# Optimization experiments

Measured on AMD Instinct MI355X. Metric: run time of the kernel, lower is better.

Reference implementation:

```python
import jax, jax.numpy as jnp
import numpy as np

NUM_HEADS = 16
NEG_INF = -1e30  # finite large negative; avoids NaN on fully-masked padded query rows


def setup_inputs() -> dict:
    key = jax.random.key(0)
    k0, k1, k2, k3 = jax.random.split(key, 4)
    B, S, E = 4, 2048, 1024
    x_padded = jax.random.normal(k0, (B, S, E), dtype=jnp.float32)
    # variable lengths in [S//2, S] so no batch row is fully empty
    seq_lengths = jax.random.randint(k1, (B,), S // 2, S + 1).astype(jnp.int32)
    Wqkv = jax.random.normal(k2, (3 * E, E), dtype=jnp.float32) * 0.02  # torch Linear weight [out,in]
    Wout = jax.random.normal(k3, (E, E), dtype=jnp.float32) * 0.02
    return {"x_padded": x_padded, "Wqkv": Wqkv, "Wout": Wout,
            "seq_lengths": seq_lengths, "window_left": 512, "window_right": 0}


def _build_mask(seq_lengths, S, window_left, window_right):
    # key-side padding mask: [B, S]
    pad = jnp.arange(S)[None, :] < seq_lengths[:, None]
    mask = pad[:, None, None, :]  # [B,1,1,S]
    if window_left >= 0 or window_right >= 0:
        i = jnp.arange(S)[:, None]
        j = jnp.arange(S)[None, :]
        win = jnp.ones((S, S), dtype=bool)
        if window_left >= 0:
            win = win & (j >= i - window_left)
        if window_right >= 0:
            win = win & (j <= i + window_right)
        mask = mask & win[None, None, :, :]
    elif (window_left, window_right) == (-1, 0):
        causal = jnp.tril(jnp.ones((S, S), dtype=bool))
        mask = mask & causal[None, None, :, :]
    return mask  # [B,1,S,S] (broadcasts over heads)


def reference(x_padded, Wqkv, Wout, seq_lengths, window_left, window_right):
    B, S, E = x_padded.shape
    H = NUM_HEADS
    D = E // H
    scale = 1.0 / jnp.sqrt(jnp.float32(D))
    qkv = x_padded @ Wqkv.T  # [B,S,3E]
    q, k, v = jnp.split(qkv, 3, axis=-1)
    q = q.reshape(B, S, H, D).transpose(0, 2, 1, 3)  # [B,H,S,D]
    k = k.reshape(B, S, H, D).transpose(0, 2, 1, 3)
    v = v.reshape(B, S, H, D).transpose(0, 2, 1, 3)
    mask = _build_mask(seq_lengths, S, window_left, window_right)
    scores = jnp.einsum("bhid,bhjd->bhij", q, k) * scale
    scores = jnp.where(mask, scores, NEG_INF)
    attn = jax.nn.softmax(scores, axis=-1)
    out = jnp.einsum("bhij,bhjd->bhid", attn, v)  # [B,H,S,D]
    out = out.transpose(0, 2, 1, 3).reshape(B, S, E)
    return out @ Wout.T
```

## Files before the change

kernel.cpp:

```cpp
#include <hip/hip_runtime.h>

typedef __bf16 bf16;
typedef __attribute__((ext_vector_type(2))) __bf16 bf16x2;
typedef __attribute__((ext_vector_type(4))) __bf16 bf16x4;
typedef __attribute__((ext_vector_type(8))) __bf16 bf16x8;
typedef __attribute__((ext_vector_type(4))) float f32x4;
typedef __attribute__((ext_vector_type(16))) float f32x16;

#define B_ 4
#define S_ 2048
#define H_ 16
#define D_ 64
#define E_ 1024

__device__ __forceinline__ int imin(int a, int b) { return a < b ? a : b; }
__device__ __forceinline__ int imax(int a, int b) { return a > b ? a : b; }

__device__ __forceinline__ void gload_lds16(const void* g, void* l) {
  __builtin_amdgcn_global_load_lds(
      (const __attribute__((address_space(1))) void*)g,
      (__attribute__((address_space(3))) void*)l, 16, 0, 0);
}

__global__ __launch_bounds__(256) void f32_to_bf16_kernel(
    const float* __restrict__ in, bf16* __restrict__ out, int n) {
  int i = (blockIdx.x * 256 + threadIdx.x) * 8;
  const int stride = gridDim.x * 256 * 8;
  for (; i < n; i += stride) {
    float4 v0 = *(const float4*)(in + i);
    float4 v1 = *(const float4*)(in + i + 4);
    bf16x8 o;
    o[0] = (bf16)v0.x; o[1] = (bf16)v0.y; o[2] = (bf16)v0.z; o[3] = (bf16)v0.w;
    o[4] = (bf16)v1.x; o[5] = (bf16)v1.y; o[6] = (bf16)v1.z; o[7] = (bf16)v1.w;
    *(bf16x8*)(out + i) = o;
  }
}

__global__ __launch_bounds__(256) void gemm_nt(
    const bf16* __restrict__ A, const bf16* __restrict__ Bm,
    int M, int N, int K, int mode,
    bf16* __restrict__ qd, bf16* __restrict__ kd, bf16* __restrict__ vtd,
    float* __restrict__ outf) {
  __shared__ __align__(16) bf16 As[128 * 64];
  __shared__ __align__(16) bf16 Bs[128 * 64];
  const int tid = threadIdx.x;
  const int wave = tid >> 6, lane = tid & 63;
  const int l15 = lane & 15, l4 = lane >> 4;
  const int tn = blockIdx.x, tm = blockIdx.y;
  const int wm = (wave >> 1) * 64, wn = (wave & 1) * 64;

  f32x4 acc[4][4];
#pragma unroll
  for (int i = 0; i < 4; ++i)
#pragma unroll
    for (int j = 0; j < 4; ++j)
#pragma unroll
      for (int r = 0; r < 4; ++r) acc[i][j][r] = 0.f;

  const bf16* Abase = A + (size_t)tm * 128 * K;
  const bf16* Bbase = Bm + (size_t)tn * 128 * K;

  for (int k0 = 0; k0 < K; k0 += 64) {
#pragma unroll
    for (int it = 0; it < 4; ++it) {
      const int gidx = it * 256 + tid;
      const int row = gidx >> 3, c = gidx & 7;
      const int csw = c ^ (row & 7);
      gload_lds16(Abase + (size_t)row * K + k0 + csw * 8,
                  As + (size_t)(it * 256 + wave * 64) * 8);
      gload_lds16(Bbase + (size_t)row * K + k0 + csw * 8,
                  Bs + (size_t)(it * 256 + wave * 64) * 8);
    }
    __syncthreads();
#pragma unroll
    for (int kc = 0; kc < 2; ++kc) {
      bf16x8 af[4], bfr[4];
#pragma unroll
      for (int i = 0; i < 4; ++i) {
        const int ra = wm + i * 16 + l15;
        af[i] = *(const bf16x8*)(As + ra * 64 + (((kc * 4 + l4) ^ (ra & 7)) * 8));
        const int rb = wn + i * 16 + l15;
        bfr[i] = *(const bf16x8*)(Bs + rb * 64 + (((kc * 4 + l4) ^ (rb & 7)) * 8));
      }
#pragma unroll
      for (int i = 0; i < 4; ++i)
#pragma unroll
        for (int j = 0; j < 4; ++j)
          acc[i][j] = __builtin_amdgcn_mfma_f32_16x16x32_bf16(af[i], bfr[j],
                                                              acc[i][j], 0, 0, 0);
    }
    __syncthreads();
  }

  if (mode == 0) {
#pragma unroll
    for (int i = 0; i < 4; ++i) {
      const int m0 = tm * 128 + wm + i * 16 + l4 * 4;
      const int b = m0 >> 11, s = m0 & (S_ - 1);
#pragma unroll
      for (int j = 0; j < 4; ++j) {
        const int n = tn * 128 + wn + j * 16 + l15;
        const int which = n >> 10;
        const int hn = n & 1023;
        const int h = hn >> 6, d = hn & 63;
        const f32x4 a = acc[i][j];
        if (which == 0) {
#pragma unroll
          for (int r = 0; r < 4; ++r)
            qd[((size_t)(b * H_ + h) * S_ + (s + r)) * D_ + d] =
                (bf16)(a[r] * 0.125f);
        } else if (which == 1) {
#pragma unroll
          for (int r = 0; r < 4; ++r)
            kd[((size_t)(b * H_ + h) * S_ + (s + r)) * D_ + d] = (bf16)a[r];
        } else {
          bf16x4 pv;
#pragma unroll
          for (int r = 0; r < 4; ++r) pv[r] = (bf16)a[r];
          *(bf16x4*)(vtd + ((size_t)(b * H_ + h) * D_ + d) * S_ + s) = pv;
        }
      }
    }
  } else {
#pragma unroll
    for (int i = 0; i < 4; ++i) {
      const int m0 = tm * 128 + wm + i * 16 + l4 * 4;
#pragma unroll
      for (int j = 0; j < 4; ++j) {
        const int n = tn * 128 + wn + j * 16 + l15;
#pragma unroll
        for (int r = 0; r < 4; ++r) outf[(size_t)(m0 + r) * N + n] = acc[i][j][r];
      }
    }
  }
}

__global__ __launch_bounds__(256) void meanv_kernel(const bf16* __restrict__ vt,
                                                    float* __restrict__ meanv) {
  __shared__ float part[256];
  const int bh = blockIdx.x;
  const int tid = threadIdx.x;
  const int d = tid & 63, seg = tid >> 6;
  const bf16* row = vt + ((size_t)bh * D_ + d) * S_ + seg * 512;
  float s = 0.f;
  for (int i = 0; i < 512; i += 8) {
    bf16x8 v = *(const bf16x8*)(row + i);
#pragma unroll
    for (int j = 0; j < 8; ++j) s += (float)v[j];
  }
  part[tid] = s;
  __syncthreads();
  if (tid < 64) {
    float t = part[tid] + part[64 + tid] + part[128 + tid] + part[192 + tid];
    meanv[(size_t)bh * D_ + tid] = t * (1.0f / (float)S_);
  }
}

__device__ __forceinline__ int pk2(float a, float b) {
  union { bf16x2 h; int i; } u;
  u.h[0] = (bf16)a; u.h[1] = (bf16)b;
  return u.i;
}

__global__ __launch_bounds__(256) void attn_kernel(
    const bf16* __restrict__ q, const bf16* __restrict__ k,
    const bf16* __restrict__ vt, const float* __restrict__ meanv,
    const int* __restrict__ seq_lengths, const int* __restrict__ wlp,
    const int* __restrict__ wrp, bf16* __restrict__ attn_out) {
  const int tid = threadIdx.x, wave = tid >> 6, lane = tid & 63;
  const int l31 = lane & 31, l5 = lane >> 5;
  const int bid = blockIdx.x;
  const int bh = bid >> 4;
  const int g = bid & 15;
  const int b = bh >> 4, h = bh & 15;
  const int q0w = g * 128 + wave * 32;
  const int seq_len = seq_lengths[b];
  const int wl = wlp[0], wr = wrp[0];

  const bf16* qbase = q + (size_t)bh * S_ * D_;
  const bf16* kbase = k + (size_t)bh * S_ * D_;
  const bf16* vtb = vt + (size_t)bh * D_ * S_;

  bf16x8 qa[4];
#pragma unroll
  for (int dg = 0; dg < 4; ++dg)
    qa[dg] = *(const bf16x8*)(qbase + (size_t)(q0w + l31) * D_ + dg * 16 + l5 * 8);

  const int hi_ = (wr >= 0) ? imin(q0w + 31 + wr, S_ - 1) : (S_ - 1);
  const int kv_end = imin(hi_ + 1, seq_len);
  const int lo_ = (wl >= 0) ? imax(0, q0w - wl) : 0;
  const int kv_begin = lo_ & ~31;

  f32x16 o0, o1;
#pragma unroll
  for (int r = 0; r < 16; ++r) { o0[r] = 0.f; o1[r] = 0.f; }
  float mrun = -1e30f, lrun = 0.f;

  for (int kt = kv_begin; kt < kv_end; kt += 32) {
    f32x16 sf;
#pragma unroll
    for (int r = 0; r < 16; ++r) sf[r] = 0.f;
#pragma unroll
    for (int dg = 0; dg < 4; ++dg) {
      bf16x8 kb = *(const bf16x8*)(kbase + (size_t)(kt + l31) * D_ + dg * 16 + l5 * 8);
      sf = __builtin_amdgcn_mfma_f32_32x32x16_bf16(kb, qa[dg], sf, 0, 0, 0);
    }

    bool allv = (kt + 31 < seq_len);
    if (wr >= 0) allv = allv && (kt + 31 <= q0w + wr);
    if (wl >= 0) allv = allv && (kt >= q0w + 31 - wl);

    float p[16];
    float tmax = -1e30f;
    if (allv) {
#pragma unroll
      for (int r = 0; r < 16; ++r) { p[r] = sf[r]; tmax = fmaxf(tmax, p[r]); }
    } else {
      const int qrow = q0w + l31;
#pragma unroll
      for (int r = 0; r < 16; ++r) {
        const int key = kt + (r & 3) + 8 * (r >> 2) + 4 * l5;
        bool valid = (key < seq_len);
        if (wr >= 0) valid = valid && (key <= qrow + wr);
        if (wl >= 0) valid = valid && (key >= qrow - wl);
        p[r] = valid ? sf[r] : -1e30f;
        tmax = fmaxf(tmax, p[r]);
      }
    }
    tmax = fmaxf(tmax, __shfl_xor(tmax, 32, 64));

    if (!__all(tmax <= mrun + 8.0f)) {
      const float mnew = fmaxf(mrun, tmax);
      const float corr = __expf(mrun - mnew);
      mrun = mnew;
      lrun *= corr;
#pragma unroll
      for (int r = 0; r < 16; ++r) { o0[r] *= corr; o1[r] *= corr; }
    }

    float lsum = 0.f;
#pragma unroll
    for (int r = 0; r < 16; ++r) {
      const float pe = (p[r] <= -1e29f) ? 0.f : __expf(p[r] - mrun);
      p[r] = pe;
      lsum += pe;
    }
    lsum += __shfl_xor(lsum, 32, 64);
    lrun += lsum;

    bf16x8 pb[2];
#pragma unroll
    for (int kg = 0; kg < 2; ++kg) {
      const int w0 = pk2(p[kg * 8 + 0], p[kg * 8 + 1]);
      const int w1 = pk2(p[kg * 8 + 2], p[kg * 8 + 3]);
      const int w2 = pk2(p[kg * 8 + 4], p[kg * 8 + 5]);
      const int w3 = pk2(p[kg * 8 + 6], p[kg * 8 + 7]);
      auto r02 = __builtin_amdgcn_permlane32_swap(w0, w2, false, false);
      auto r13 = __builtin_amdgcn_permlane32_swap(w1, w3, false, false);
      union { int i[4]; bf16x8 v; } u;
      u.i[0] = r02[0]; u.i[1] = r13[0]; u.i[2] = r02[1]; u.i[3] = r13[1];
      pb[kg] = u.v;
    }

#pragma unroll
    for (int kg = 0; kg < 2; ++kg) {
      bf16x8 v0 = *(const bf16x8*)(vtb + (size_t)(l31) * S_ + kt + kg * 16 + l5 * 8);
      bf16x8 v1 = *(const bf16x8*)(vtb + (size_t)(32 + l31) * S_ + kt + kg * 16 + l5 * 8);
      o0 = __builtin_amdgcn_mfma_f32_32x32x16_bf16(v0, pb[kg], o0, 0, 0, 0);
      o1 = __builtin_amdgcn_mfma_f32_32x32x16_bf16(v1, pb[kg], o1, 0, 0, 0);
    }
  }

  const int qrow = q0w + l31;
  bf16* outp = attn_out + ((size_t)(b * S_ + qrow)) * E_ + h * 64;
  if (lrun > 0.f) {
    const float inv = 1.0f / lrun;
#pragma unroll
    for (int dg2 = 0; dg2 < 2; ++dg2) {
      const f32x16& o = dg2 ? o1 : o0;
#pragma unroll
      for (int rg = 0; rg < 4; ++rg) {
        const int d0 = dg2 * 32 + 8 * rg + 4 * l5;
        bf16x4 ov;
#pragma unroll
        for (int j = 0; j < 4; ++j) ov[j] = (bf16)(o[rg * 4 + j] * inv);
        *(bf16x4*)(outp + d0) = ov;
      }
    }
  } else {
    const float* mv = meanv + (size_t)bh * D_;
#pragma unroll
    for (int dg2 = 0; dg2 < 2; ++dg2)
#pragma unroll
      for (int rg = 0; rg < 4; ++rg) {
        const int d0 = dg2 * 32 + 8 * rg + 4 * l5;
        bf16x4 ov;
#pragma unroll
        for (int j = 0; j < 4; ++j) ov[j] = (bf16)mv[d0 + j];
        *(bf16x4*)(outp + d0) = ov;
      }
  }
}

extern "C" void kernel_launch(void* const* d_in, const int* in_sizes, int n_in,
                              void* d_out, int out_size, void* d_ws, size_t ws_size,
                              hipStream_t stream) {
  const float* x = (const float*)d_in[0];
  const float* Wqkv = (const float*)d_in[1];
  const float* Wout = (const float*)d_in[2];
  const int* seq_lengths = (const int*)d_in[3];
  const int* wl = (const int*)d_in[4];
  const int* wr = (const int*)d_in[5];
  float* out = (float*)d_out;

  char* ws = (char*)d_ws;
  bf16* xb = (bf16*)ws;      ws += (size_t)8192 * 1024 * 2;
  bf16* wqkvb = (bf16*)ws;   ws += (size_t)3072 * 1024 * 2;
  bf16* woutb = (bf16*)ws;   ws += (size_t)1024 * 1024 * 2;
  bf16* qd = (bf16*)ws;      ws += (size_t)B_ * H_ * S_ * D_ * 2;
  bf16* kd = (bf16*)ws;      ws += (size_t)B_ * H_ * S_ * D_ * 2;
  bf16* vtd = (bf16*)ws;     ws += (size_t)B_ * H_ * S_ * D_ * 2;
  bf16* attn = (bf16*)ws;    ws += (size_t)8192 * 1024 * 2;
  float* meanv = (float*)ws; ws += (size_t)B_ * H_ * D_ * 4;

  f32_to_bf16_kernel<<<2048, 256, 0, stream>>>(x, xb, 8192 * 1024);
  f32_to_bf16_kernel<<<768, 256, 0, stream>>>(Wqkv, wqkvb, 3072 * 1024);
  f32_to_bf16_kernel<<<512, 256, 0, stream>>>(Wout, woutb, 1024 * 1024);

  gemm_nt<<<dim3(24, 64), 256, 0, stream>>>(xb, wqkvb, 8192, 3072, 1024, 0,
                                            qd, kd, vtd, nullptr);
  meanv_kernel<<<64, 256, 0, stream>>>(vtd, meanv);
  attn_kernel<<<1024, 256, 0, stream>>>(qd, kd, vtd, meanv, seq_lengths, wl, wr,
                                        attn);
  gemm_nt<<<dim3(8, 64), 256, 0, stream>>>(attn, woutb, 8192, 1024, 1024, 1,
                                           nullptr, nullptr, nullptr, out);
}
```

Baseline: 194.2 us.

## Split KV range across two waves per query tile with LDS merge and prefetch

The attention kernel now gives each 32-row query tile to a 128-thread block whose two waves take alternating KV tiles. The partial softmax states (max, sum, output accumulators) are merged through shared memory at the end. K tiles are prefetched one iteration ahead and V loads are hoisted before the softmax to hide load latency. Block IDs are remapped to spread heads across XCDs. This raises parallelism and latency hiding, at the cost of an LDS merge, a barrier, and more blocks.

Result: no change. 192.5 us (-0.9%).

```diff
diff --git a/kernel.cpp b/kernel.cpp
--- a/kernel.cpp
+++ b/kernel.cpp
@@ -162,18 +162,21 @@
   return u.i;
 }
 
-__global__ __launch_bounds__(256) void attn_kernel(
+__global__ __launch_bounds__(128) void attn_kernel(
     const bf16* __restrict__ q, const bf16* __restrict__ k,
     const bf16* __restrict__ vt, const float* __restrict__ meanv,
     const int* __restrict__ seq_lengths, const int* __restrict__ wlp,
     const int* __restrict__ wrp, bf16* __restrict__ attn_out) {
+  __shared__ float Lm[64], Ll[64];
+  __shared__ float Lo[32][64];
   const int tid = threadIdx.x, wave = tid >> 6, lane = tid & 63;
   const int l31 = lane & 31, l5 = lane >> 5;
-  const int bid = blockIdx.x;
-  const int bh = bid >> 4;
-  const int g = bid & 15;
+  const int bid0 = blockIdx.x;
+  const int bid = (bid0 & 7) * 512 + (bid0 >> 3);
+  const int bh = bid >> 6;
+  const int g = bid & 63;
   const int b = bh >> 4, h = bh & 15;
-  const int q0w = g * 128 + wave * 32;
+  const int q0w = g * 32;
   const int seq_len = seq_lengths[b];
   const int wl = wlp[0], wr = wrp[0];
 
@@ -190,21 +193,41 @@
   const int kv_end = imin(hi_ + 1, seq_len);
   const int lo_ = (wl >= 0) ? imax(0, q0w - wl) : 0;
   const int kv_begin = lo_ & ~31;
+  const int span = kv_end - kv_begin;
+  const int nt = (span > 0) ? ((span + 31) >> 5) : 0;
 
   f32x16 o0, o1;
 #pragma unroll
   for (int r = 0; r < 16; ++r) { o0[r] = 0.f; o1[r] = 0.f; }
   float mrun = -1e30f, lrun = 0.f;
 
-  for (int kt = kv_begin; kt < kv_end; kt += 32) {
+  int kt0 = kv_begin + wave * 32;
+  if (wave >= nt) kt0 = kv_begin;
+  bf16x8 kreg[4];
+#pragma unroll
+  for (int dg = 0; dg < 4; ++dg)
+    kreg[dg] = *(const bf16x8*)(kbase + (size_t)(kt0 + l31) * D_ + dg * 16 + l5 * 8);
+
+  for (int t = wave; t < nt; t += 2) {
+    const int kt = kv_begin + t * 32;
     f32x16 sf;
 #pragma unroll
     for (int r = 0; r < 16; ++r) sf[r] = 0.f;
 #pragma unroll
-    for (int dg = 0; dg < 4; ++dg) {
-      bf16x8 kb = *(const bf16x8*)(kbase + (size_t)(kt + l31) * D_ + dg * 16 + l5 * 8);
-      sf = __builtin_amdgcn_mfma_f32_32x32x16_bf16(kb, qa[dg], sf, 0, 0, 0);
-    }
+    for (int dg = 0; dg < 4; ++dg)
+      sf = __builtin_amdgcn_mfma_f32_32x32x16_bf16(kreg[dg], qa[dg], sf, 0, 0, 0);
+
+    bf16x8 vreg[4];
+#pragma unroll
+    for (int kg = 0; kg < 2; ++kg) {
+      vreg[kg * 2 + 0] = *(const bf16x8*)(vtb + (size_t)(l31) * S_ + kt + kg * 16 + l5 * 8);
+      vreg[kg * 2 + 1] = *(const bf16x8*)(vtb + (size_t)(32 + l31) * S_ + kt + kg * 16 + l5 * 8);
+    }
+    int ktn = kv_begin + (t + 2) * 32;
+    if (t + 2 >= nt) ktn = kv_begin;
+#pragma unroll
+    for (int dg = 0; dg < 4; ++dg)
+      kreg[dg] = *(const bf16x8*)(kbase + (size_t)(ktn + l31) * D_ + dg * 16 + l5 * 8);
 
     bool allv = (kt + 31 < seq_len);
     if (wr >= 0) allv = allv && (kt + 31 <= q0w + wr);
@@ -264,17 +287,37 @@
 
 #pragma unroll
     for (int kg = 0; kg < 2; ++kg) {
-      bf16x8 v0 = *(const bf16x8*)(vtb + (size_t)(l31) * S_ + kt + kg * 16 + l5 * 8);
-      bf16x8 v1 = *(const bf16x8*)(vtb + (size_t)(32 + l31) * S_ + kt + kg * 16 + l5 * 8);
-      o0 = __builtin_amdgcn_mfma_f32_32x32x16_bf16(v0, pb[kg], o0, 0, 0, 0);
-      o1 = __builtin_amdgcn_mfma_f32_32x32x16_bf16(v1, pb[kg], o1, 0, 0, 0);
-    }
+      o0 = __builtin_amdgcn_mfma_f32_32x32x16_bf16(vreg[kg * 2 + 0], pb[kg], o0, 0, 0, 0);
+      o1 = __builtin_amdgcn_mfma_f32_32x32x16_bf16(vreg[kg * 2 + 1], pb[kg], o1, 0, 0, 0);
+    }
+  }
+
+  if (wave == 1) {
+    Lm[lane] = mrun;
+    Ll[lane] = lrun;
+#pragma unroll
+    for (int r = 0; r < 16; ++r) {
+      Lo[r][lane] = o0[r];
+      Lo[16 + r][lane] = o1[r];
+    }
+  }
+  __syncthreads();
+  if (wave == 1) return;
+
+  const float m2 = Lm[lane], l2 = Ll[lane];
+  const float ms = fmaxf(mrun, m2);
+  const float w1 = __expf(mrun - ms), w2 = __expf(m2 - ms);
+  const float ls = lrun * w1 + l2 * w2;
+#pragma unroll
+  for (int r = 0; r < 16; ++r) {
+    o0[r] = o0[r] * w1 + Lo[r][lane] * w2;
+    o1[r] = o1[r] * w1 + Lo[16 + r][lane] * w2;
   }
 
   const int qrow = q0w + l31;
   bf16* outp = attn_out + ((size_t)(b * S_ + qrow)) * E_ + h * 64;
-  if (lrun > 0.f) {
-    const float inv = 1.0f / lrun;
+  if (ls > 0.f) {
+    const float inv = 1.0f / ls;
 #pragma unroll
     for (int dg2 = 0; dg2 < 2; ++dg2) {
       const f32x16& o = dg2 ? o1 : o0;
@@ -330,7 +373,7 @@
   gemm_nt<<<dim3(24, 64), 256, 0, stream>>>(xb, wqkvb, 8192, 3072, 1024, 0,
                                             qd, kd, vtd, nullptr);
   meanv_kernel<<<64, 256, 0, stream>>>(vtd, meanv);
-  attn_kernel<<<1024, 256, 0, stream>>>(qd, kd, vtd, meanv, seq_lengths, wl, wr,
+  attn_kernel<<<4096, 128, 0, stream>>>(qd, kd, vtd, meanv, seq_lengths, wl, wr,
                                         attn);
   gemm_nt<<<dim3(8, 64), 256, 0, stream>>>(attn, woutb, 8192, 1024, 1024, 1,
                                            nullptr, nullptr, nullptr, out);
```
